# Performance work log

Hardware: AMD Instinct MI355X
Metric: run time of the kernel (lower is better)

The kernel has to match this reference:

```python
import jax, jax.numpy as jnp
import numpy as np

# ---- model dims (from init_kwargs) ----
N_C, K_C, L_C = 128, 64, 8
D, H, N_DEC = 256, 8, 6
DH = D // H                      # 32 per-head dim
M = int(DH * np.log(DH))         # 110 random features (performer default)
SEQ = L_C * (2 * N_C - K_C)      # 1536 tokens
BS = 32
EPS = 1e-4                       # performer softmax-kernel epsilon


def _ortho(rng, m, d):
    # gaussian orthogonal random features, scaling=0 (performer default)
    blocks = []
    for _ in range(int(np.ceil(m / d))):
        q, _ = np.linalg.qr(rng.standard_normal((d, d)))
        blocks.append(q.T)
    mat = np.concatenate(blocks, 0)[:m]
    mult = np.linalg.norm(rng.standard_normal((m, d)), axis=1)
    return (mult[:, None] * mat).astype(np.float32)


def _xavier(rng, shape):
    fan_in, fan_out = shape[-2], shape[-1]
    lim = np.sqrt(6.0 / (fan_in + fan_out))
    return jnp.asarray(rng.uniform(-lim, lim, size=shape).astype(np.float32))


def setup_inputs() -> dict:
    key = jax.random.key(0)
    k1, k2, k3, k4 = jax.random.split(key, 4)
    rng = np.random.default_rng(0)
    L2 = (2, N_DEC)  # [decoder / decoder_T, layer]
    proj = np.stack([np.stack([_ortho(rng, M, DH) for _ in range(N_DEC)])
                     for _ in range(2)])
    return {
        'magnitude':   jax.random.normal(k1, (BS, L_C, N_C), jnp.float32),
        'syndrome':    jax.random.normal(k2, (BS, L_C, N_C - K_C), jnp.float32),
        'magnitude_T': jax.random.normal(k3, (BS, N_C, L_C), jnp.float32),
        'syndrome_T':  jax.random.normal(k4, (BS, N_C - K_C, L_C), jnp.float32),
        'src_embed':   _xavier(rng, (SEQ, D)),
        'src_embed_T': _xavier(rng, (SEQ, D)),
        'ln1_s': jnp.ones(L2 + (D,)),  'ln1_b': jnp.zeros(L2 + (D,)),
        'Wq': _xavier(rng, L2 + (D, D)), 'bq': jnp.zeros(L2 + (D,)),
        'Wk': _xavier(rng, L2 + (D, D)), 'bk': jnp.zeros(L2 + (D,)),
        'Wv': _xavier(rng, L2 + (D, D)), 'bv': jnp.zeros(L2 + (D,)),
        'Wo': _xavier(rng, L2 + (D, D)), 'bo': jnp.zeros(L2 + (D,)),
        'proj': jnp.asarray(proj),                       # [2,N_DEC,M,DH] buffers
        'ln2_s': jnp.ones(L2 + (D,)),  'ln2_b': jnp.zeros(L2 + (D,)),
        'W1': _xavier(rng, L2 + (D, 2 * D)), 'b1': jnp.zeros(L2 + (2 * D,)),
        'W2': _xavier(rng, L2 + (2 * D, D)), 'b2': jnp.zeros(L2 + (D,)),
        'final_w': _xavier(rng, (D, 1)), 'final_b': jnp.zeros((1,)),
        'out_w': _xavier(rng, (SEQ, N_C * L_C)), 'out_b': jnp.zeros((N_C * L_C,)),
    }


def _ln(y, s, b):
    mu = jnp.mean(y, -1, keepdims=True)
    var = jnp.mean((y - mu) ** 2, -1, keepdims=True)
    return (y - mu) * jax.lax.rsqrt(var + 1e-5) * s + b


def _softmax_kernel(x, proj, is_query):
    # x: [b,h,n,dh], proj: [m,dh] -> phi(x): [b,h,n,m]
    nrm = x.shape[-1] ** -0.25
    ratio = proj.shape[0] ** -0.5
    xd = jnp.einsum('bhnd,md->bhnm', x * nrm, proj)
    diag = jnp.sum(x * x, -1, keepdims=True) * 0.5 * (nrm * nrm)
    if is_query:
        stab = jax.lax.stop_gradient(jnp.max(xd, -1, keepdims=True))
    else:
        stab = jax.lax.stop_gradient(jnp.max(xd, (-2, -1), keepdims=True))
    return ratio * (jnp.exp(xd - diag - stab) + EPS)


PKEYS = ('ln1_s', 'ln1_b', 'Wq', 'bq', 'Wk', 'bk', 'Wv', 'bv', 'Wo', 'bo',
         'proj', 'ln2_s', 'ln2_b', 'W1', 'b1', 'W2', 'b2')


def _block(x, p):
    b, n, d = x.shape

    def attn(y):
        h = _ln(y, p['ln1_s'], p['ln1_b'])
        q, k, v = [(h @ W + bb).reshape(b, n, H, DH).transpose(0, 2, 1, 3)
                   for W, bb in ((p['Wq'], p['bq']), (p['Wk'], p['bk']), (p['Wv'], p['bv']))]
        qp = _softmax_kernel(q, p['proj'], True)   # [b,h,n,m]
        kp = _softmax_kernel(k, p['proj'], False)
        d_inv = 1.0 / jnp.einsum('bhnm,bhm->bhn', qp, kp.sum(-2))
        ctx = jnp.einsum('bhnm,bhnd->bhmd', kp, v)          # [b,h,m,dh]
        o = jnp.einsum('bhnm,bhmd,bhn->bhnd', qp, ctx, d_inv)
        return o.transpose(0, 2, 1, 3).reshape(b, n, d) @ p['Wo'] + p['bo']

    def ff(y):
        h = _ln(y, p['ln2_s'], p['ln2_b'])
        return jax.nn.gelu(h @ p['W1'] + p['b1'], approximate=False) @ p['W2'] + p['b2']

    # reversible stream with x1 = x2 = x, merged by mean of the two streams
    y1 = x + attn(x)
    y2 = x + ff(y1)
    return 0.5 * (y1 + y2)


def _forward(magnitude, syndrome, magnitude_T, syndrome_T, src_embed, src_embed_T,
             params, final_w, final_b, out_w, out_b):
    bs = magnitude.shape[0]
    emb = jnp.concatenate([magnitude, syndrome], -1).reshape(bs, SEQ, 1) * src_embed[None]
    emb_T = jnp.concatenate([magnitude_T, syndrome_T], 1).reshape(bs, SEQ, 1) * src_embed_T[None]
    for i in range(N_DEC):
        emb = _block(emb, {k: params[k][0, i] for k in PKEYS})
    for i in range(N_DEC):
        emb_T = _block(emb_T, {k: params[k][1, i] for k in PKEYS})
    # transpose-merge of the T stream
    emb_T = emb_T.reshape(bs, 2 * N_C - K_C, L_C, D).transpose(0, 2, 1, 3).reshape(bs, SEQ, D)
    emb = emb + emb_T
    z = (emb @ final_w + final_b)[..., 0]     # [bs, SEQ]
    return z @ out_w + out_b                  # [bs, n*l]


def reference(magnitude, syndrome, magnitude_T, syndrome_T, src_embed, src_embed_T,
              ln1_s, ln1_b, Wq, bq, Wk, bk, Wv, bv, Wo, bo, proj, ln2_s, ln2_b,
              W1, b1, W2, b2, final_w, final_b, out_w, out_b):
    params = dict(ln1_s=ln1_s, ln1_b=ln1_b, Wq=Wq, bq=bq, Wk=Wk, bk=bk, Wv=Wv, bv=bv,
                  Wo=Wo, bo=bo, proj=proj, ln2_s=ln2_s, ln2_b=ln2_b,
                  W1=W1, b1=b1, W2=W2, b2=b2)
    return _forward(magnitude, syndrome, magnitude_T, syndrome_T,
                    src_embed, src_embed_T, params, final_w, final_b, out_w, out_b)
```

## Files before the change

### kernel.cpp

```cpp
#include <hip/hip_runtime.h>
#include <hip/hip_bf16.h>
#include <math.h>

#define BSZ 32
#define SEQ 1536
#define DM 256
#define NH 8
#define DH 32
#define MF 110
#define NL 6
#define RB (BSZ*SEQ)
#define NCH 12
#define CH (SEQ/NCH)
#define QKVW 768

#define NRM 0.4204482076268573f
#define HALF_NRM2 0.08838834764831845f
#define RATIO 0.09534625892455922f
#define PEPS 1e-4f

typedef unsigned short u16;
using short8v = __attribute__((ext_vector_type(8))) short;
using f32x4   = __attribute__((ext_vector_type(4))) float;

#define GLOAD_LDS16(g, l) __builtin_amdgcn_global_load_lds( \
    (const __attribute__((address_space(1))) void*)(g), \
    (__attribute__((address_space(3))) void*)(l), 16, 0, 0)

__device__ __forceinline__ float wredsum(float v){
  #pragma unroll
  for (int o=32;o;o>>=1) v += __shfl_xor(v,o);
  return v;
}
__device__ __forceinline__ u16 f2bf(float x){
  unsigned u = __float_as_uint(x);
  return (u16)((u + 0x7FFFu + ((u>>16)&1u)) >> 16);
}
__device__ __forceinline__ float b2f(u16 h){
  return __uint_as_float(((unsigned)h)<<16);
}

__global__ __launch_bounds__(256) void sentinel_k(float* __restrict__ out, int n, float v)
{
  int i = blockIdx.x*256 + threadIdx.x;
  if (i < n) out[i] = v;
}

__global__ __launch_bounds__(256) void zero_k(float* __restrict__ p, int n)
{
  int i = blockIdx.x*256 + threadIdx.x;
  if (i < n) p[i] = 0.f;
}

__global__ __launch_bounds__(256) void wtrans_k(
    const float* __restrict__ src, u16* __restrict__ dst,
    int K, int N, size_t dstStride)
{
  int l = blockIdx.z;
  const float* s = src + (size_t)l*K*N;
  u16* d = dst + (size_t)l*dstStride;
  __shared__ float t[32][33];
  int k0 = blockIdx.y*32, n0 = blockIdx.x*32;
  int tx = threadIdx.x & 31, ty = threadIdx.x >> 5;
  #pragma unroll
  for (int i=0;i<32;i+=8) t[ty+i][tx] = s[(size_t)(k0+ty+i)*N + n0+tx];
  __syncthreads();
  #pragma unroll
  for (int i=0;i<32;i+=8) d[(size_t)(n0+ty+i)*K + k0+tx] = f2bf(t[tx][ty+i]);
}

__global__ __launch_bounds__(256) void bpack_k(
    const float* __restrict__ bq, const float* __restrict__ bk,
    const float* __restrict__ bv, float* __restrict__ dst)
{
  int l = blockIdx.x, t = threadIdx.x;
  dst[(size_t)l*QKVW + t]       = bq[(size_t)l*DM + t];
  dst[(size_t)l*QKVW + 256 + t] = bk[(size_t)l*DM + t];
  dst[(size_t)l*QKVW + 512 + t] = bv[(size_t)l*DM + t];
}

__global__ __launch_bounds__(256) void projcvt_k(
    const float* __restrict__ proj, u16* __restrict__ dst)
{
  int wi = blockIdx.x;
  for (int s = threadIdx.x; s < 112*32; s += 256){
    int m = s >> 5, dd = s & 31;
    float v = (m < MF) ? NRM*proj[(size_t)wi*MF*32 + (size_t)m*32 + dd] : 0.f;
    dst[(size_t)wi*112*32 + s] = f2bf(v);
  }
}

__global__ __launch_bounds__(256) void embed_k(
    const float* __restrict__ mag, const float* __restrict__ syn,
    const float* __restrict__ magT, const float* __restrict__ synT,
    const float* __restrict__ se, const float* __restrict__ seT,
    u16* __restrict__ X, int s)
{
  int tid = threadIdx.x; int w = tid>>6; int lane = tid&63;
  int row = blockIdx.x*4 + w;
  int b = row / SEQ, t = row % SEQ;
  float val; const float* sep;
  if (!s) {
    int l = t / 192, c = t % 192;
    val = (c < 128) ? mag[((size_t)b*8 + l)*128 + c]
                    : syn[((size_t)b*8 + l)*64 + (c-128)];
    sep = se;
  } else {
    int r = t >> 3, l = t & 7;
    val = (r < 128) ? magT[((size_t)b*128 + r)*8 + l]
                    : synT[((size_t)b*64 + (r-128))*8 + l];
    sep = seT;
  }
  float4 e = *(const float4*)&sep[(size_t)t*DM + lane*4];
  ushort4 o;
  o.x = f2bf(val*e.x); o.y = f2bf(val*e.y);
  o.z = f2bf(val*e.z); o.w = f2bf(val*e.w);
  *(ushort4*)&X[(size_t)row*DM + lane*4] = o;
}

__global__ __launch_bounds__(256) void lnb_k(
    const u16* __restrict__ in, u16* __restrict__ out,
    const float* __restrict__ sc, const float* __restrict__ sb)
{
  int tid=threadIdx.x, w=tid>>6, lane=tid&63;
  size_t row = (size_t)blockIdx.x*4 + w;
  const ushort4 h = *(const ushort4*)&in[row*DM + lane*4];
  float vx=b2f(h.x), vy=b2f(h.y), vz=b2f(h.z), vw=b2f(h.w);
  float sum = vx+vy+vz+vw;
  sum = wredsum(sum);
  float mu = sum * (1.f/256.f);
  float dx=vx-mu, dy=vy-mu, dz=vz-mu, dw=vw-mu;
  float vs = dx*dx+dy*dy+dz*dz+dw*dw;
  vs = wredsum(vs);
  float rstd = rsqrtf(vs*(1.f/256.f) + 1e-5f);
  float4 s4 = *(const float4*)&sc[lane*4];
  float4 b4 = *(const float4*)&sb[lane*4];
  ushort4 o;
  o.x = f2bf(dx*rstd*s4.x+b4.x); o.y = f2bf(dy*rstd*s4.y+b4.y);
  o.z = f2bf(dz*rstd*s4.z+b4.z); o.w = f2bf(dw*rstd*s4.w+b4.w);
  *(ushort4*)&out[row*DM + lane*4] = o;
}

__global__ __launch_bounds__(256) void mgemm_k(
    const u16* __restrict__ A, const u16* __restrict__ Wt,
    const float* __restrict__ bias, void* __restrict__ Cout,
    const void* __restrict__ R1, const void* __restrict__ R2,
    int K, int N, int EPI)
{
  __shared__ u16 As[128*32];
  __shared__ u16 Bs[128*32];
  const int tid = threadIdx.x;
  const int lane = tid & 63, w = tid >> 6;
  const int wr = w >> 1, wc = w & 1;
  const int nwg = gridDim.x*gridDim.y;
  const int lin = blockIdx.y*gridDim.x + blockIdx.x;
  const int cpx = nwg >> 3;
  const int swz = (lin & 7)*cpx + (lin >> 3);
  const int bx = swz % gridDim.x, by = swz / gridDim.x;
  const int r0 = by*128, c0 = bx*128;

  f32x4 acc[4][4];
  #pragma unroll
  for (int m=0;m<4;m++){
    #pragma unroll
    for (int n=0;n<4;n++) acc[m][n] = (f32x4){0.f,0.f,0.f,0.f};
  }
  const int srow = lane >> 2;
  const int klog = (lane & 3) ^ ((srow >> 1) & 3);
  const int frow = lane & 15;
  const int rph  = (lane >> 4) ^ ((frow >> 1) & 3);

  for (int k0 = 0; k0 < K; k0 += 32){
    GLOAD_LDS16(&A [(size_t)(r0 + w*32      + srow)*K + k0 + klog*8], &As[(w*32     )*32]);
    GLOAD_LDS16(&A [(size_t)(r0 + w*32 + 16 + srow)*K + k0 + klog*8], &As[(w*32 + 16)*32]);
    GLOAD_LDS16(&Wt[(size_t)(c0 + w*32      + srow)*K + k0 + klog*8], &Bs[(w*32     )*32]);
    GLOAD_LDS16(&Wt[(size_t)(c0 + w*32 + 16 + srow)*K + k0 + klog*8], &Bs[(w*32 + 16)*32]);
    __syncthreads();
    short8v a[4], bq[4];
    #pragma unroll
    for (int m=0;m<4;m++)
      a[m] = *(const short8v*)&As[(wr*64 + m*16 + frow)*32 + rph*8];
    #pragma unroll
    for (int n=0;n<4;n++)
      bq[n] = *(const short8v*)&Bs[(wc*64 + n*16 + frow)*32 + rph*8];
    #pragma unroll
    for (int m=0;m<4;m++){
      #pragma unroll
      for (int n=0;n<4;n++)
        acc[m][n] = __builtin_amdgcn_mfma_f32_16x16x32_bf16(a[m], bq[n], acc[m][n], 0,0,0);
    }
    __syncthreads();
  }
  const int cb = c0 + wc*64 + (lane&15);
  const int rb = r0 + wr*64 + (lane>>4)*4;
  #pragma unroll
  for (int m=0;m<4;m++){
    #pragma unroll
    for (int n=0;n<4;n++){
      int c = cb + n*16;
      float bb = bias[c];
      #pragma unroll
      for (int i=0;i<4;i++){
        int r = rb + m*16 + i;
        size_t off = (size_t)r*N + c;
        float v = acc[m][n][i] + bb;
        if (EPI == 0) {
          ((u16*)Cout)[off] = f2bf(v);
        } else if (EPI == 1) {
          ((u16*)Cout)[off] = f2bf(v + b2f(((const u16*)R1)[off]));
        } else if (EPI == 2) {
          v = 0.5f*v*(1.f+erff(v*0.70710678118654752f));
          ((u16*)Cout)[off] = f2bf(v);
        } else {
          ((u16*)Cout)[off] = f2bf(0.5f*(b2f(((const u16*)R1)[off]) + b2f(((const u16*)R2)[off]) + v));
        }
      }
    }
  }
}

__global__ __launch_bounds__(256) void ctxacc_k(
    const u16* __restrict__ QKV, const u16* __restrict__ projb,
    u16* __restrict__ part, float* __restrict__ svb, float* __restrict__ stabb)
{
  const int h = blockIdx.x, b = blockIdx.y, ch = blockIdx.z;
  const int tid = threadIdx.x, w = tid>>6, lane = tid&63;
  const int bh = b*NH + h;
  const int l15 = lane & 15, g = lane >> 4;
  __shared__ __align__(16) u16 et_l[128*128];
  __shared__ __align__(16) u16 vt_l[48*128];
  __shared__ float red_l[4];

  const size_t pbase = ((size_t)ch*256 + bh)*MF*36;
  const size_t sbase = ((size_t)ch*256 + bh)*32;
  const u16* Kb = QKV + ((size_t)b*SEQ + ch*CH)*QKVW + 256 + h*32;
  const u16* Vb = QKV + ((size_t)b*SEQ + ch*CH)*QKVW + 512 + h*32;

  for (int u = tid; u < 512; u += 256){
    int r = u >> 2, d0 = (u & 3)*8;
    short8v vv = *(const short8v*)&Vb[(size_t)r*QKVW + d0];
    #pragma unroll
    for (int j=0;j<8;j++){
      int d = d0 + j;
      vt_l[d*128 + (((r>>3) ^ (d&15))<<3) + (r&7)] = (u16)vv[j];
    }
  }
  for (int e = tid; e < 16*128; e += 256){
    int d = 32 + (e>>7), r = e & 127;
    vt_l[d*128 + (((r>>3) ^ (d&15))<<3) + (r&7)] = (d==32) ? (u16)0x3F80 : (u16)0;
    int m = 112 + (e>>7);
    et_l[m*128 + (((r>>3) ^ (m&15))<<3) + (r&7)] = (m==112) ? (u16)0x3F80 : (u16)0;
  }

  short8v pf[7];
  #pragma unroll
  for (int j=0;j<7;j++)
    pf[j] = *(const short8v*)&projb[(j*16 + l15)*32 + g*8];
  f32x4 xd[2][7];
  float ssf[2];
  #pragma unroll
  for (int t=0;t<2;t++){
    short8v kf = *(const short8v*)&Kb[(size_t)(w*32 + t*16 + l15)*QKVW + g*8];
    float ss = 0.f;
    #pragma unroll
    for (int j=0;j<8;j++){ float q = b2f((u16)kf[j]); ss += q*q; }
    ss += __shfl_xor(ss, 16); ss += __shfl_xor(ss, 32);
    ssf[t] = ss;
    #pragma unroll
    for (int j=0;j<7;j++)
      xd[t][j] = __builtin_amdgcn_mfma_f32_16x16x32_bf16(kf, pf[j], (f32x4){0.f,0.f,0.f,0.f}, 0,0,0);
  }
  float mx = -1e30f;
  #pragma unroll
  for (int t=0;t<2;t++){
    #pragma unroll
    for (int j=0;j<7;j++){
      if (j==6 && l15 >= 14) continue;
      #pragma unroll
      for (int i=0;i<4;i++) mx = fmaxf(mx, xd[t][j][i]);
    }
  }
  #pragma unroll
  for (int o=32;o;o>>=1) mx = fmaxf(mx, __shfl_xor(mx,o));
  if (lane == 0) red_l[w] = mx;
  __syncthreads();
  const float stab = fmaxf(fmaxf(red_l[0],red_l[1]), fmaxf(red_l[2],red_l[3]));
  if (tid == 0) stabb[(size_t)ch*256 + bh] = stab;

  #pragma unroll
  for (int t=0;t<2;t++){
    int rbase = w*32 + t*16 + g*4;
    int slot = rbase >> 3;
    float dg[4];
    #pragma unroll
    for (int i=0;i<4;i++)
      dg[i] = HALF_NRM2 * __shfl(ssf[t], (lane & 48) | (g*4 + i));
    #pragma unroll
    for (int j=0;j<7;j++){
      int m = j*16 + l15;
      ushort4 pk;
      u16* pkp = &pk.x;
      #pragma unroll
      for (int i=0;i<4;i++){
        float e = (j==6 && l15>=14) ? 0.f : __expf(xd[t][j][i] - dg[i] - stab);
        pkp[i] = f2bf(e);
      }
      *(ushort4*)&et_l[m*128 + ((slot ^ (m&15))<<3) + (rbase & 7)] = pk;
    }
  }
  __syncthreads();

  #pragma unroll
  for (int mi=0; mi<2; mi++){
    int mt = w + mi*4;
    f32x4 a0 = (f32x4){0.f,0.f,0.f,0.f}, a1 = a0, a2 = a0;
    #pragma unroll
    for (int ks=0; ks<4; ks++){
      int sl = g + 4*ks;
      short8v ea = *(const short8v*)&et_l[(mt*16 + l15)*128 + ((sl ^ l15)<<3)];
      short8v v0 = *(const short8v*)&vt_l[(     l15)*128 + ((sl ^ l15)<<3)];
      short8v v1 = *(const short8v*)&vt_l[(16 + l15)*128 + ((sl ^ l15)<<3)];
      short8v v2 = *(const short8v*)&vt_l[(32 + l15)*128 + ((sl ^ l15)<<3)];
      a0 = __builtin_amdgcn_mfma_f32_16x16x32_bf16(ea, v0, a0, 0,0,0);
      a1 = __builtin_amdgcn_mfma_f32_16x16x32_bf16(ea, v1, a1, 0,0,0);
      a2 = __builtin_amdgcn_mfma_f32_16x16x32_bf16(ea, v2, a2, 0,0,0);
    }
    #pragma unroll
    for (int i=0;i<4;i++){
      int m = mt*16 + g*4 + i;
      if (m < MF){
        u16* pp = part + pbase + (size_t)m*36;
        pp[l15]      = f2bf(a0[i]);
        pp[16 + l15] = f2bf(a1[i]);
        if (l15 == 0) pp[32] = f2bf(a2[i]);
      } else if (m == 112){
        svb[sbase + l15]      = a0[i];
        svb[sbase + 16 + l15] = a1[i];
      }
    }
  }
}

__global__ __launch_bounds__(256) void ctxred_k(
    const u16* __restrict__ part, const float* __restrict__ svb,
    const float* __restrict__ stabb,
    u16* __restrict__ ctxTb, float* __restrict__ ksumg)
{
  int t = blockIdx.x*256 + threadIdx.x;
  int d = t % 36;
  if (d >= 33) return;
  int bhm = t / 36;
  int bh = bhm / MF, m = bhm % MF;
  float gstab = -1e30f;
  float st[NCH];
  #pragma unroll
  for (int ch=0; ch<NCH; ch++){
    st[ch] = stabb[(size_t)ch*256 + bh];
    gstab = fmaxf(gstab, st[ch]);
  }
  float s = 0.f;
  #pragma unroll
  for (int ch=0; ch<NCH; ch++){
    size_t base = ((size_t)ch*256 + bh)*MF*36 + (size_t)m*36;
    s += b2f(part[base + d]) * __expf(st[ch] - gstab);
  }
  if (d < 32){
    float svtot = 0.f;
    #pragma unroll
    for (int ch=0; ch<NCH; ch++) svtot += svb[((size_t)ch*256 + bh)*32 + d];
    ctxTb[(size_t)bh*4096 + (size_t)d*128 + m] = f2bf(RATIO*(s + PEPS*svtot));
  } else {
    ksumg[(size_t)bh*112 + m] = RATIO*(s + PEPS*(float)SEQ);
  }
}

__global__ __launch_bounds__(256) void oattn_k(
    const u16* __restrict__ QKV, const u16* __restrict__ projb,
    const u16* __restrict__ ctxTb, const float* __restrict__ ksumg,
    u16* __restrict__ Og)
{
  const int blk = blockIdx.x, h = blockIdx.y, b = blockIdx.z;
  const int tid = threadIdx.x, wv = tid>>6, lane = tid&63;
  const int bh = b*NH + h;
  __shared__ __align__(16) u16 proj_l[112*40];
  __shared__ __align__(16) u16 ctx_l[32*136];
  __shared__ float ksum_l[112];
  __shared__ float diag_l[4][16];
  __shared__ __align__(16) u16 phi_l[4][16*136];

  for (int s = tid; s < 448; s += 256){
    int r = s>>2, k8 = (s&3)*8;
    *(short8v*)&proj_l[r*40 + k8] = *(const short8v*)&projb[r*32 + k8];
  }
  for (int s = tid; s < 512; s += 256){
    int r = s>>4, m8 = (s&15)*8;
    *(short8v*)&ctx_l[r*136 + m8] = *(const short8v*)&ctxTb[(size_t)bh*4096 + r*128 + m8];
  }
  if (tid < 112) ksum_l[tid] = ksumg[(size_t)bh*112 + tid];
  for (int s = tid; s < 4*16*24; s += 256){
    int wvx = s/(16*24); int rem = s - wvx*16*24;
    phi_l[wvx][(rem/24)*136 + 112 + (rem%24)] = 0;
  }
  __syncthreads();

  const int l15 = lane & 15, g = lane >> 4;
  const u16* qbase = QKV + (size_t)b*SEQ*QKVW + h*32;
  const int rowblk = blk*256;

  for (int it = 0; it < 4; it++){
    const int r0 = rowblk + it*64 + wv*16;
    short8v qa = *(const short8v*)&qbase[(size_t)(r0 + l15)*QKVW + g*8];
    float ss = 0.f;
    #pragma unroll
    for (int j=0;j<8;j++){ float q = b2f((u16)qa[j]); ss += q*q; }
    ss += __shfl_xor(ss, 16); ss += __shfl_xor(ss, 32);
    if (lane < 16) diag_l[wv][lane] = HALF_NRM2 * ss;
    f32x4 xd[7];
    #pragma unroll
    for (int j=0;j<7;j++){
      short8v pf = *(const short8v*)&proj_l[(j*16 + l15)*40 + g*8];
      xd[j] = __builtin_amdgcn_mfma_f32_16x16x32_bf16(qa, pf, (f32x4){0.f,0.f,0.f,0.f}, 0,0,0);
    }
    float rden[4];
    #pragma unroll
    for (int i=0;i<4;i++){
      float mx = xd[0][i];
      #pragma unroll
      for (int j=1;j<7;j++) mx = fmaxf(mx, xd[j][i]);
      mx = fmaxf(mx, __shfl_xor(mx,1)); mx = fmaxf(mx, __shfl_xor(mx,2));
      mx = fmaxf(mx, __shfl_xor(mx,4)); mx = fmaxf(mx, __shfl_xor(mx,8));
      float dg = diag_l[wv][g*4+i];
      float dsum = 0.f;
      #pragma unroll
      for (int j=0;j<7;j++){
        float ph = RATIO*(__expf(xd[j][i] - dg - mx) + PEPS);
        xd[j][i] = ph;
        dsum += ph * ksum_l[l15 + 16*j];
      }
      dsum += __shfl_xor(dsum,1); dsum += __shfl_xor(dsum,2);
      dsum += __shfl_xor(dsum,4); dsum += __shfl_xor(dsum,8);
      rden[i] = 1.f / dsum;
      #pragma unroll
      for (int j=0;j<7;j++)
        phi_l[wv][(g*4+i)*136 + l15 + 16*j] = f2bf(xd[j][i]);
    }
    f32x4 o0 = (f32x4){0.f,0.f,0.f,0.f}, o1 = (f32x4){0.f,0.f,0.f,0.f};
    #pragma unroll
    for (int ks=0; ks<4; ks++){
      short8v af = *(const short8v*)&phi_l[wv][l15*136 + g*8 + ks*32];
      short8v b0 = *(const short8v*)&ctx_l[l15*136 + g*8 + ks*32];
      short8v b1 = *(const short8v*)&ctx_l[(16+l15)*136 + g*8 + ks*32];
      o0 = __builtin_amdgcn_mfma_f32_16x16x32_bf16(af, b0, o0, 0,0,0);
      o1 = __builtin_amdgcn_mfma_f32_16x16x32_bf16(af, b1, o1, 0,0,0);
    }
    u16* orow = Og + ((size_t)b*SEQ + r0)*DM + h*32;
    #pragma unroll
    for (int i=0;i<4;i++){
      int r = g*4 + i;
      orow[(size_t)r*DM + l15]      = f2bf(o0[i] * rden[i]);
      orow[(size_t)r*DM + 16 + l15] = f2bf(o1[i] * rden[i]);
    }
  }
}

__global__ __launch_bounds__(256) void zacc_k(
    const u16* __restrict__ X, const float* __restrict__ fw,
    const float* __restrict__ fb, float* __restrict__ Z, int mode)
{
  int tid=threadIdx.x, w=tid>>6, lane=tid&63;
  int row = blockIdx.x*4 + w;
  int b = row/SEQ, t = row%SEQ;
  int tt = t;
  if (mode == 1) {
    int l = t/192, r = t%192;
    tt = r*8 + l;
  }
  const ushort4 xh = *(const ushort4*)&X[((size_t)b*SEQ + tt)*DM + lane*4];
  const float4 f4 = *(const float4*)&fw[lane*4];
  float ssum = b2f(xh.x)*f4.x + b2f(xh.y)*f4.y + b2f(xh.z)*f4.z + b2f(xh.w)*f4.w;
  ssum = wredsum(ssum);
  if (lane==0) {
    if (mode == 0) Z[row] = ssum + fb[0];
    else           Z[row] += ssum;
  }
}

__global__ __launch_bounds__(256) void out_k(
    const float* __restrict__ Z, const float* __restrict__ outw,
    const float* __restrict__ outb, float* __restrict__ out)
{
  const int c = blockIdx.x*64 + (threadIdx.x & 63);
  const int tg = threadIdx.x >> 6;
  const int b = blockIdx.y;
  __shared__ float zs[SEQ];
  __shared__ float red[4][64];
  for (int t = threadIdx.x; t < SEQ; t += 256) zs[t] = Z[(size_t)b*SEQ + t];
  __syncthreads();
  float acc = 0.f;
  const int t0 = tg*384;
  for (int t = t0; t < t0+384; t++) acc += zs[t] * outw[(size_t)t*1024 + c];
  red[tg][threadIdx.x & 63] = acc;
  __syncthreads();
  if (tg == 0)
    out[(size_t)b*1024 + c] = red[0][c & 63] + red[1][c & 63] + red[2][c & 63] + red[3][c & 63] + outb[c];
}

extern "C" void kernel_launch(void* const* d_in, const int* in_sizes, int n_in,
                              void* d_out, int out_size, void* d_ws, size_t ws_size,
                              hipStream_t stream) {
  (void)in_sizes; (void)n_in;
  const float* mag  = (const float*)d_in[0];
  const float* syn  = (const float*)d_in[1];
  const float* magT = (const float*)d_in[2];
  const float* synT = (const float*)d_in[3];
  const float* se   = (const float*)d_in[4];
  const float* seT  = (const float*)d_in[5];
  const float* ln1s = (const float*)d_in[6];
  const float* ln1b = (const float*)d_in[7];
  const float* Wq   = (const float*)d_in[8];
  const float* bq   = (const float*)d_in[9];
  const float* Wk   = (const float*)d_in[10];
  const float* bk   = (const float*)d_in[11];
  const float* Wv   = (const float*)d_in[12];
  const float* bv   = (const float*)d_in[13];
  const float* Wo   = (const float*)d_in[14];
  const float* bo   = (const float*)d_in[15];
  const float* proj = (const float*)d_in[16];
  const float* ln2s = (const float*)d_in[17];
  const float* ln2b = (const float*)d_in[18];
  const float* W1   = (const float*)d_in[19];
  const float* b1   = (const float*)d_in[20];
  const float* W2   = (const float*)d_in[21];
  const float* b2   = (const float*)d_in[22];
  const float* fw   = (const float*)d_in[23];
  const float* fb   = (const float*)d_in[24];
  const float* outw = (const float*)d_in[25];
  const float* outb = (const float*)d_in[26];
  float* out = (float*)d_out;

  char* base = (char*)d_ws;
  const size_t PANEL = (size_t)RB*DM;
  size_t off = 0;
  u16*  Xh    = (u16*)(base + off);   off += PANEL*4;
  float* Y1   = (float*)(base + off); off += PANEL*4;
  u16*  Hb    = (u16*)(base + off);   off += PANEL*2;
  u16*  QKVb  = (u16*)(base + off);   off += PANEL*2*3;
  u16*  Wts   = (u16*)(base + off);   off += (size_t)12*524288*2;
  u16*  CTXTb = (u16*)(base + off);   off += (size_t)256*4096*2;
  float* KSb  = (float*)(base + off); off += (size_t)256*112*4;
  float* SVb  = (float*)(base + off); off += (size_t)NCH*256*32*4;
  float* STb  = (float*)(base + off); off += (size_t)NCH*256*4;
  float* BQKV = (float*)(base + off); off += (size_t)12*QKVW*4;
  u16*  PROJB = (u16*)(base + off);   off += (size_t)12*112*32*2;
  float* Zb   = (float*)(base + off); off += (size_t)BSZ*SEQ*4;
  if (ws_size < off) {
    float v = 100000.0f + (float)(ws_size >> 20);
    sentinel_k<<<dim3((out_size+255)/256), 256, 0, stream>>>(out, out_size, v);
    return;
  }
  u16*  PARTb = (u16*)Y1;
  u16*  Y1h   = (u16*)Y1;
  const size_t WST = 524288;

  wtrans_k<<<dim3(8,8,12),  256, 0, stream>>>(Wq, Wts + 0,      256, 256, WST);
  wtrans_k<<<dim3(8,8,12),  256, 0, stream>>>(Wk, Wts + 65536,  256, 256, WST);
  wtrans_k<<<dim3(8,8,12),  256, 0, stream>>>(Wv, Wts + 131072, 256, 256, WST);
  wtrans_k<<<dim3(8,8,12),  256, 0, stream>>>(Wo, Wts + 196608, 256, 256, WST);
  wtrans_k<<<dim3(16,8,12), 256, 0, stream>>>(W1, Wts + 262144, 256, 512, WST);
  wtrans_k<<<dim3(8,16,12), 256, 0, stream>>>(W2, Wts + 393216, 512, 256, WST);
  bpack_k<<<dim3(12), 256, 0, stream>>>(bq, bk, bv, BQKV);
  projcvt_k<<<dim3(12), 256, 0, stream>>>(proj, PROJB);
  zero_k<<<dim3((256*4096*2/4 + 255)/256), 256, 0, stream>>>((float*)CTXTb, 256*4096*2/4);
  zero_k<<<dim3((256*112 + 255)/256), 256, 0, stream>>>(KSb, 256*112);

  for (int s=0; s<2; s++){
    embed_k<<<dim3(RB/4), 256, 0, stream>>>(mag, syn, magT, synT, se, seT, Xh, s);
    for (int l=0; l<NL; l++){
      int wi = s*NL + l;
      const u16* Wqkvt = Wts + (size_t)wi*WST;
      const u16* Wot = Wqkvt + 196608;
      const u16* W1t = Wqkvt + 262144;
      const u16* W2t = Wqkvt + 393216;
      const u16* pprojb = PROJB + (size_t)wi*112*32;

      lnb_k<<<dim3(RB/4), 256, 0, stream>>>(Xh, Hb, ln1s + (size_t)wi*DM, ln1b + (size_t)wi*DM);
      mgemm_k<<<dim3(6,384), 256, 0, stream>>>(Hb, Wqkvt, BQKV + (size_t)wi*QKVW, QKVb, nullptr, nullptr, 256, QKVW, 0);
      ctxacc_k<<<dim3(NH,BSZ,NCH), 256, 0, stream>>>(QKVb, pprojb, PARTb, SVb, STb);
      ctxred_k<<<dim3(MF*36), 256, 0, stream>>>(PARTb, SVb, STb, CTXTb, KSb);
      oattn_k<<<dim3(SEQ/256, NH, BSZ), 256, 0, stream>>>(QKVb, pprojb, CTXTb, KSb, Hb);
      mgemm_k<<<dim3(2,384), 256, 0, stream>>>(Hb, Wot, bo + (size_t)wi*DM, Y1h, Xh, nullptr, 256, 256, 1);
      lnb_k<<<dim3(RB/4), 256, 0, stream>>>(Y1h, Hb, ln2s + (size_t)wi*DM, ln2b + (size_t)wi*DM);
      mgemm_k<<<dim3(4,384), 256, 0, stream>>>(Hb, W1t, b1 + (size_t)wi*512, QKVb, nullptr, nullptr, 256, 512, 2);
      mgemm_k<<<dim3(2,384), 256, 0, stream>>>(QKVb, W2t, b2 + (size_t)wi*DM, Xh, Xh, Y1h, 512, 256, 3);
    }
    zacc_k<<<dim3(RB/4), 256, 0, stream>>>(Xh, fw, fb, Zb, s);
  }

  out_k<<<dim3(16, BSZ), 256, 0, stream>>>(Zb, outw, outb, out);
}
```

Baseline: 3.085 ms.

## Fuse LayerNorm into the full-row epilogue of the Wo and W2 GEMMs

Adds a GEMM kernel whose tiles are 64 rows by the full 256 columns. This lets the residual add and the following LayerNorm (ln2 after Wo, next layer's ln1 after W2) run in the epilogue with in-register row reductions. Standalone LayerNorm launches drop to one per stream, removing a full read and write of the activation per fused norm. The trade-off is a narrower tile: A-fragment reuse is lower, each wave issues more LDS reads per MFMA, and register pressure is higher, so the GEMMs may run less efficiently.

```diff
diff --git a/kernel.cpp b/kernel.cpp
--- a/kernel.cpp
+++ b/kernel.cpp
@@ -144,7 +144,6 @@
 __global__ __launch_bounds__(256) void mgemm_k(
     const u16* __restrict__ A, const u16* __restrict__ Wt,
     const float* __restrict__ bias, void* __restrict__ Cout,
-    const void* __restrict__ R1, const void* __restrict__ R2,
     int K, int N, int EPI)
 {
   __shared__ u16 As[128*32];
@@ -204,16 +203,93 @@
         int r = rb + m*16 + i;
         size_t off = (size_t)r*N + c;
         float v = acc[m][n][i] + bb;
-        if (EPI == 0) {
-          ((u16*)Cout)[off] = f2bf(v);
-        } else if (EPI == 1) {
-          ((u16*)Cout)[off] = f2bf(v + b2f(((const u16*)R1)[off]));
-        } else if (EPI == 2) {
-          v = 0.5f*v*(1.f+erff(v*0.70710678118654752f));
-          ((u16*)Cout)[off] = f2bf(v);
-        } else {
-          ((u16*)Cout)[off] = f2bf(0.5f*(b2f(((const u16*)R1)[off]) + b2f(((const u16*)R2)[off]) + v));
-        }
+        if (EPI == 2) v = 0.5f*v*(1.f+erff(v*0.70710678118654752f));
+        ((u16*)Cout)[off] = f2bf(v);
+      }
+    }
+  }
+}
+
+__global__ __launch_bounds__(256) void mgemmln_k(
+    const u16* __restrict__ A, const u16* __restrict__ Wt,
+    const float* __restrict__ bias, u16* __restrict__ Cout,
+    const u16* __restrict__ R1, const u16* __restrict__ R2,
+    const float* __restrict__ lsc, const float* __restrict__ lsb,
+    u16* __restrict__ Hout, int K, int EPI)
+{
+  __shared__ u16 As[64*32];
+  __shared__ u16 Bs[256*32];
+  __shared__ float bss[256], scs[256], sbs[256];
+  const int tid = threadIdx.x;
+  const int lane = tid & 63, wv = tid >> 6;
+  const int nwg = gridDim.x;
+  const int lin = blockIdx.x;
+  const int cpx = nwg >> 3;
+  const int swz = (lin & 7)*cpx + (lin >> 3);
+  const int r0 = swz*64;
+
+  bss[tid] = bias[tid];
+  if (lsc){ scs[tid] = lsc[tid]; sbs[tid] = lsb[tid]; }
+
+  f32x4 acc[16];
+  #pragma unroll
+  for (int n=0;n<16;n++) acc[n] = (f32x4){0.f,0.f,0.f,0.f};
+  const int srow = lane >> 2;
+  const int klog = (lane & 3) ^ ((srow >> 1) & 3);
+  const int frow = lane & 15;
+  const int rph  = (lane >> 4) ^ ((frow >> 1) & 3);
+  const int l15 = lane & 15;
+
+  for (int k0 = 0; k0 < K; k0 += 32){
+    GLOAD_LDS16(&A[(size_t)(r0 + wv*16 + srow)*K + k0 + klog*8], &As[(wv*16)*32]);
+    #pragma unroll
+    for (int q=0;q<4;q++)
+      GLOAD_LDS16(&Wt[(size_t)(wv*64 + q*16 + srow)*K + k0 + klog*8], &Bs[(wv*64 + q*16)*32]);
+    __syncthreads();
+    short8v a = *(const short8v*)&As[(wv*16 + frow)*32 + rph*8];
+    #pragma unroll
+    for (int n=0;n<16;n++){
+      short8v bq = *(const short8v*)&Bs[(n*16 + frow)*32 + rph*8];
+      acc[n] = __builtin_amdgcn_mfma_f32_16x16x32_bf16(a, bq, acc[n], 0,0,0);
+    }
+    __syncthreads();
+  }
+  const int rb = r0 + wv*16 + (lane>>4)*4;
+  #pragma unroll
+  for (int n=0;n<16;n++){
+    int c = n*16 + l15;
+    float bb = bss[c];
+    #pragma unroll
+    for (int i=0;i<4;i++){
+      size_t off = (size_t)(rb + i)*DM + c;
+      float v = acc[n][i] + bb;
+      if (EPI == 1) v = v + b2f(R1[off]);
+      else          v = 0.5f*(b2f(R1[off]) + b2f(R2[off]) + v);
+      u16 hh = f2bf(v);
+      Cout[off] = hh;
+      acc[n][i] = b2f(hh);
+    }
+  }
+  if (lsc){
+    #pragma unroll
+    for (int i=0;i<4;i++){
+      float s = 0.f;
+      #pragma unroll
+      for (int n=0;n<16;n++) s += acc[n][i];
+      s += __shfl_xor(s,1); s += __shfl_xor(s,2);
+      s += __shfl_xor(s,4); s += __shfl_xor(s,8);
+      float mu = s * (1.f/256.f);
+      float vs = 0.f;
+      #pragma unroll
+      for (int n=0;n<16;n++){ float d = acc[n][i] - mu; vs += d*d; }
+      vs += __shfl_xor(vs,1); vs += __shfl_xor(vs,2);
+      vs += __shfl_xor(vs,4); vs += __shfl_xor(vs,8);
+      float rstd = rsqrtf(vs*(1.f/256.f) + 1e-5f);
+      #pragma unroll
+      for (int n=0;n<16;n++){
+        int c = n*16 + l15;
+        size_t off = (size_t)(rb + i)*DM + c;
+        Hout[off] = f2bf((acc[n][i] - mu)*rstd*scs[c] + sbs[c]);
       }
     }
   }
@@ -582,16 +658,20 @@
       const u16* W1t = Wqkvt + 262144;
       const u16* W2t = Wqkvt + 393216;
       const u16* pprojb = PROJB + (size_t)wi*112*32;
-
-      lnb_k<<<dim3(RB/4), 256, 0, stream>>>(Xh, Hb, ln1s + (size_t)wi*DM, ln1b + (size_t)wi*DM);
-      mgemm_k<<<dim3(6,384), 256, 0, stream>>>(Hb, Wqkvt, BQKV + (size_t)wi*QKVW, QKVb, nullptr, nullptr, 256, QKVW, 0);
+      const bool last = (l == NL-1);
+
+      if (l == 0)
+        lnb_k<<<dim3(RB/4), 256, 0, stream>>>(Xh, Hb, ln1s + (size_t)wi*DM, ln1b + (size_t)wi*DM);
+      mgemm_k<<<dim3(6,384), 256, 0, stream>>>(Hb, Wqkvt, BQKV + (size_t)wi*QKVW, QKVb, 256, QKVW, 0);
       ctxacc_k<<<dim3(NH,BSZ,NCH), 256, 0, stream>>>(QKVb, pprojb, PARTb, SVb, STb);
       ctxred_k<<<dim3(MF*36), 256, 0, stream>>>(PARTb, SVb, STb, CTXTb, KSb);
       oattn_k<<<dim3(SEQ/256, NH, BSZ), 256, 0, stream>>>(QKVb, pprojb, CTXTb, KSb, Hb);
-      mgemm_k<<<dim3(2,384), 256, 0, stream>>>(Hb, Wot, bo + (size_t)wi*DM, Y1h, Xh, nullptr, 256, 256, 1);
-      lnb_k<<<dim3(RB/4), 256, 0, stream>>>(Y1h, Hb, ln2s + (size_t)wi*DM, ln2b + (size_t)wi*DM);
-      mgemm_k<<<dim3(4,384), 256, 0, stream>>>(Hb, W1t, b1 + (size_t)wi*512, QKVb, nullptr, nullptr, 256, 512, 2);
-      mgemm_k<<<dim3(2,384), 256, 0, stream>>>(QKVb, W2t, b2 + (size_t)wi*DM, Xh, Xh, Y1h, 512, 256, 3);
+      mgemmln_k<<<dim3(768), 256, 0, stream>>>(Hb, Wot, bo + (size_t)wi*DM, Y1h, Xh, nullptr,
+                                               ln2s + (size_t)wi*DM, ln2b + (size_t)wi*DM, Hb, 256, 1);
+      mgemm_k<<<dim3(4,384), 256, 0, stream>>>(Hb, W1t, b1 + (size_t)wi*512, QKVb, 256, 512, 2);
+      mgemmln_k<<<dim3(768), 256, 0, stream>>>(QKVb, W2t, b2 + (size_t)wi*DM, Xh, Xh, Y1h,
+                                               last ? nullptr : ln1s + (size_t)(wi+1)*DM,
+                                               last ? nullptr : ln1b + (size_t)(wi+1)*DM, Hb, 512, 3);
     }
     zacc_k<<<dim3(RB/4), 256, 0, stream>>>(Xh, fw, fb, Zb, s);
   }
```

After: 3.425 ms. 11.0% more time.

## Fuse LayerNorm into the QKV and FFN1 GEMM prologue

Applied to the files above, without the earlier changes.

Removes the standalone LayerNorm kernels ahead of the QKV and W1 GEMMs. The new GEMM kernel loads the full 128x256 A tile into LDS, computes per-row mean and rstd there, normalizes in place, then runs the MFMA loop over K with only B streamed. This saves a write and re-read of the normalized activations and two launches per layer. In exchange it uses a 64KB LDS A tile, which cuts occupancy, and recomputes the LayerNorm redundantly in every column block (6 or 4 times per row).

```diff
diff --git a/kernel.cpp b/kernel.cpp
--- a/kernel.cpp
+++ b/kernel.cpp
@@ -118,29 +118,6 @@
   *(ushort4*)&X[(size_t)row*DM + lane*4] = o;
 }
 
-__global__ __launch_bounds__(256) void lnb_k(
-    const u16* __restrict__ in, u16* __restrict__ out,
-    const float* __restrict__ sc, const float* __restrict__ sb)
-{
-  int tid=threadIdx.x, w=tid>>6, lane=tid&63;
-  size_t row = (size_t)blockIdx.x*4 + w;
-  const ushort4 h = *(const ushort4*)&in[row*DM + lane*4];
-  float vx=b2f(h.x), vy=b2f(h.y), vz=b2f(h.z), vw=b2f(h.w);
-  float sum = vx+vy+vz+vw;
-  sum = wredsum(sum);
-  float mu = sum * (1.f/256.f);
-  float dx=vx-mu, dy=vy-mu, dz=vz-mu, dw=vw-mu;
-  float vs = dx*dx+dy*dy+dz*dz+dw*dw;
-  vs = wredsum(vs);
-  float rstd = rsqrtf(vs*(1.f/256.f) + 1e-5f);
-  float4 s4 = *(const float4*)&sc[lane*4];
-  float4 b4 = *(const float4*)&sb[lane*4];
-  ushort4 o;
-  o.x = f2bf(dx*rstd*s4.x+b4.x); o.y = f2bf(dy*rstd*s4.y+b4.y);
-  o.z = f2bf(dz*rstd*s4.z+b4.z); o.w = f2bf(dw*rstd*s4.w+b4.w);
-  *(ushort4*)&out[row*DM + lane*4] = o;
-}
-
 __global__ __launch_bounds__(256) void mgemm_k(
     const u16* __restrict__ A, const u16* __restrict__ Wt,
     const float* __restrict__ bias, void* __restrict__ Cout,
@@ -214,6 +191,134 @@
         } else {
           ((u16*)Cout)[off] = f2bf(0.5f*(b2f(((const u16*)R1)[off]) + b2f(((const u16*)R2)[off]) + v));
         }
+      }
+    }
+  }
+}
+
+__global__ __launch_bounds__(256) void mgemmlnA_k(
+    const u16* __restrict__ A, const u16* __restrict__ Wt,
+    const float* __restrict__ lsc, const float* __restrict__ lsb,
+    const float* __restrict__ bias, u16* __restrict__ Cout,
+    int N, int EPI)
+{
+  __shared__ u16 Af[128*256];
+  __shared__ u16 Bs[128*32];
+  __shared__ float mu_s[128], rs_s[128];
+  __shared__ float sc_s[256], sb_s[256];
+  const int tid = threadIdx.x;
+  const int lane = tid & 63, w = tid >> 6;
+  const int wr = w >> 1, wc = w & 1;
+  const int nwg = gridDim.x*gridDim.y;
+  const int lin = blockIdx.y*gridDim.x + blockIdx.x;
+  const int cpx = nwg >> 3;
+  const int swz = (lin & 7)*cpx + (lin >> 3);
+  const int bx = swz % gridDim.x, by = swz / gridDim.x;
+  const int r0 = by*128, c0 = bx*128;
+
+  sc_s[tid] = lsc[tid];
+  sb_s[tid] = lsb[tid];
+
+  {
+    const int lrow_in = lane >> 5;
+    const int l31 = lane & 31;
+    const int sl = l31 >> 2;
+    #pragma unroll
+    for (int p = 0; p < 16; p++){
+      int lrow = w*32 + p*2 + lrow_in;
+      int kl = (l31 & 3) ^ ((lrow >> 1) & 3);
+      GLOAD_LDS16(&A[(size_t)(r0 + lrow)*256 + sl*32 + kl*8], &Af[(size_t)(w*32 + p*2)*256]);
+    }
+  }
+  __syncthreads();
+
+  {
+    const int row = tid >> 1, half = tid & 1;
+    float sum = 0.f;
+    #pragma unroll
+    for (int c=0;c<16;c++){
+      short8v v = *(const short8v*)&Af[(size_t)row*256 + half*128 + c*8];
+      #pragma unroll
+      for (int j=0;j<8;j++) sum += b2f((u16)v[j]);
+    }
+    sum += __shfl_xor(sum, 1);
+    float mu = sum * (1.f/256.f);
+    float vs = 0.f;
+    #pragma unroll
+    for (int c=0;c<16;c++){
+      short8v v = *(const short8v*)&Af[(size_t)row*256 + half*128 + c*8];
+      #pragma unroll
+      for (int j=0;j<8;j++){ float d = b2f((u16)v[j]) - mu; vs += d*d; }
+    }
+    vs += __shfl_xor(vs, 1);
+    float rs = rsqrtf(vs*(1.f/256.f) + 1e-5f);
+    if (half == 0){ mu_s[row] = mu; rs_s[row] = rs; }
+    __syncthreads();
+    const float muv = mu_s[row], rsv = rs_s[row];
+    const int swb = (row >> 1) & 3;
+    #pragma unroll
+    for (int c=0;c<16;c++){
+      int off = half*128 + c*8;
+      int sl = off >> 5;
+      int sp = (off >> 3) & 3;
+      int kbase = sl*32 + (sp ^ swb)*8;
+      short8v v = *(const short8v*)&Af[(size_t)row*256 + off];
+      short8v o;
+      #pragma unroll
+      for (int j=0;j<8;j++){
+        int k = kbase + j;
+        o[j] = (short)f2bf((b2f((u16)v[j]) - muv)*rsv*sc_s[k] + sb_s[k]);
+      }
+      *(short8v*)&Af[(size_t)row*256 + off] = o;
+    }
+  }
+  __syncthreads();
+
+  f32x4 acc[4][4];
+  #pragma unroll
+  for (int m=0;m<4;m++){
+    #pragma unroll
+    for (int n=0;n<4;n++) acc[m][n] = (f32x4){0.f,0.f,0.f,0.f};
+  }
+  const int srow = lane >> 2;
+  const int klog = (lane & 3) ^ ((srow >> 1) & 3);
+  const int frow = lane & 15;
+  const int rph  = (lane >> 4) ^ ((frow >> 1) & 3);
+
+  for (int k0 = 0; k0 < 256; k0 += 32){
+    GLOAD_LDS16(&Wt[(size_t)(c0 + w*32      + srow)*256 + k0 + klog*8], &Bs[(w*32     )*32]);
+    GLOAD_LDS16(&Wt[(size_t)(c0 + w*32 + 16 + srow)*256 + k0 + klog*8], &Bs[(w*32 + 16)*32]);
+    __syncthreads();
+    short8v a[4], bq[4];
+    #pragma unroll
+    for (int m=0;m<4;m++)
+      a[m] = *(const short8v*)&Af[(size_t)(wr*64 + m*16 + frow)*256 + k0 + rph*8];
+    #pragma unroll
+    for (int n=0;n<4;n++)
+      bq[n] = *(const short8v*)&Bs[(wc*64 + n*16 + frow)*32 + rph*8];
+    #pragma unroll
+    for (int m=0;m<4;m++){
+      #pragma unroll
+      for (int n=0;n<4;n++)
+        acc[m][n] = __builtin_amdgcn_mfma_f32_16x16x32_bf16(a[m], bq[n], acc[m][n], 0,0,0);
+    }
+    __syncthreads();
+  }
+  const int cb = c0 + wc*64 + (lane&15);
+  const int rb = r0 + wr*64 + (lane>>4)*4;
+  #pragma unroll
+  for (int m=0;m<4;m++){
+    #pragma unroll
+    for (int n=0;n<4;n++){
+      int c = cb + n*16;
+      float bb = bias[c];
+      #pragma unroll
+      for (int i=0;i<4;i++){
+        int r = rb + m*16 + i;
+        size_t off = (size_t)r*N + c;
+        float v = acc[m][n][i] + bb;
+        if (EPI == 2) v = 0.5f*v*(1.f+erff(v*0.70710678118654752f));
+        Cout[off] = f2bf(v);
       }
     }
   }
@@ -583,14 +688,16 @@
       const u16* W2t = Wqkvt + 393216;
       const u16* pprojb = PROJB + (size_t)wi*112*32;
 
-      lnb_k<<<dim3(RB/4), 256, 0, stream>>>(Xh, Hb, ln1s + (size_t)wi*DM, ln1b + (size_t)wi*DM);
-      mgemm_k<<<dim3(6,384), 256, 0, stream>>>(Hb, Wqkvt, BQKV + (size_t)wi*QKVW, QKVb, nullptr, nullptr, 256, QKVW, 0);
+      mgemmlnA_k<<<dim3(6,384), 256, 0, stream>>>(Xh, Wqkvt,
+          ln1s + (size_t)wi*DM, ln1b + (size_t)wi*DM,
+          BQKV + (size_t)wi*QKVW, QKVb, QKVW, 0);
       ctxacc_k<<<dim3(NH,BSZ,NCH), 256, 0, stream>>>(QKVb, pprojb, PARTb, SVb, STb);
       ctxred_k<<<dim3(MF*36), 256, 0, stream>>>(PARTb, SVb, STb, CTXTb, KSb);
       oattn_k<<<dim3(SEQ/256, NH, BSZ), 256, 0, stream>>>(QKVb, pprojb, CTXTb, KSb, Hb);
       mgemm_k<<<dim3(2,384), 256, 0, stream>>>(Hb, Wot, bo + (size_t)wi*DM, Y1h, Xh, nullptr, 256, 256, 1);
-      lnb_k<<<dim3(RB/4), 256, 0, stream>>>(Y1h, Hb, ln2s + (size_t)wi*DM, ln2b + (size_t)wi*DM);
-      mgemm_k<<<dim3(4,384), 256, 0, stream>>>(Hb, W1t, b1 + (size_t)wi*512, QKVb, nullptr, nullptr, 256, 512, 2);
+      mgemmlnA_k<<<dim3(4,384), 256, 0, stream>>>(Y1h, W1t,
+          ln2s + (size_t)wi*DM, ln2b + (size_t)wi*DM,
+          b1 + (size_t)wi*512, QKVb, 512, 2);
       mgemm_k<<<dim3(2,384), 256, 0, stream>>>(QKVb, W2t, b2 + (size_t)wi*DM, Xh, Xh, Y1h, 512, 256, 3);
     }
     zacc_k<<<dim3(RB/4), 256, 0, stream>>>(Xh, fw, fb, Zb, s);
```

After: 3.968 ms. 28.6% more time.
